# Performance work log

Hardware: AMD Instinct MI355X
Metric: run time of the kernel (lower is better)

Reference implementation:

```python
import jax, jax.numpy as jnp
import numpy as np

B, T, E = 512, 12, 1024   # batch, channels/seq, embed_dim
NH, HS = 8, 128           # num_heads, head_size (head_size=128 hard-coded in source)
H = NH * HS               # sLSTM hidden = 1024 (== E)


def _layer_norm(x, g, b, eps=1e-5):
    mu = x.mean(-1, keepdims=True)
    var = x.var(-1, keepdims=True)
    return (x - mu) * jax.lax.rsqrt(var + eps) * g + b


def _conv1d_same(x, w, b):
    # x: (B, C, L), w: (O, I, K) odd K, 'same' padding, stride 1
    k = w.shape[-1]
    p = (k - 1) // 2
    y = jax.lax.conv_general_dilated(x, w, (1,), [(p, p)],
                                     dimension_numbers=('NCH', 'OIH', 'NCH'))
    return y + b[None, :, None]


def setup_inputs():
    key = jax.random.key(0)
    ks = jax.random.split(key, 16)
    s = 0.02
    def nrm(k, shape, scale=s):
        return jax.random.normal(k, shape, jnp.float32) * scale
    return {
        'x': jax.random.normal(ks[0], (B, T, E), jnp.float32),
        'ln_g': jnp.ones((E,), jnp.float32), 'ln_b': jnp.zeros((E,), jnp.float32),
        'fc1_w': nrm(ks[1], (12, 12, 3)), 'fc1_b': jnp.zeros((12,), jnp.float32),
        'fc2_w': nrm(ks[2], (12, 12)), 'fc2_b': jnp.zeros((12,), jnp.float32),
        'conv1_w': nrm(ks[3], (48, 12, 3)), 'conv1_b': jnp.zeros((48,), jnp.float32),
        'conv2_w': nrm(ks[4], (12, 48, 3)), 'conv2_b': jnp.zeros((12,), jnp.float32),
        'xl_ln_g': jnp.ones((E,), jnp.float32), 'xl_ln_b': jnp.zeros((E,), jnp.float32),
        'Wg': nrm(ks[5], (E, 4 * H)), 'bg': jnp.zeros((4 * H,), jnp.float32),
        'Rg': nrm(ks[6], (NH, 4 * HS, HS)),
        'gn_g': jnp.ones((H,), jnp.float32), 'gn_b': jnp.zeros((H,), jnp.float32),
        'upl_w': nrm(ks[7], (H, H)), 'upl_b': jnp.zeros((H,), jnp.float32),
        'upr_w': nrm(ks[8], (H, H)), 'upr_b': jnp.zeros((H,), jnp.float32),
        'down_w': nrm(ks[9], (H, E)), 'down_b': jnp.zeros((E,), jnp.float32),
    }


def _slstm_block(x, xl_ln_g, xl_ln_b, Wg, bg, Rg, gn_g, gn_b,
                 upl_w, upl_b, upr_w, upr_b, down_w, down_b):
    # Stabilized multi-head sLSTM block: pre-LN -> sLSTM recurrence (exp i/f gates
    # with max-stabilizer m), per-head GroupNorm, gated up/down proj (proj_factor=1),
    # residual. Recurrent weights are block-diagonal per head (NH, 4*HS, HS).
    xn = _layer_norm(x, xl_ln_g, xl_ln_b)
    gx = jnp.einsum('bte,eg->btg', xn, Wg) + bg            # (B,T,4H) input gate pre-acts
    gx = jnp.swapaxes(gx, 0, 1)                            # (T,B,4H)

    def step(carry, g_t):
        h, c, n, m = carry                                 # each (B,NH,HS)
        rec = jnp.einsum('bnh,ngh->bng', h, Rg)            # (B,NH,4HS)
        g = g_t.reshape(g_t.shape[0], NH, 4 * HS) + rec
        z_, i_, f_, o_ = jnp.split(g, 4, axis=-1)
        z = jnp.tanh(z_)
        o = jax.nn.sigmoid(o_)
        m_new = jnp.maximum(f_ + m, i_)                    # log-space stabilizer
        i = jnp.exp(i_ - m_new)
        f = jnp.exp(f_ + m - m_new)
        c = f * c + i * z
        n = f * n + i
        h = o * (c / n)
        return (h, c, n, m_new), h

    zero = jnp.zeros((x.shape[0], NH, HS), x.dtype)
    _, hseq = jax.lax.scan(step, (zero, zero, zero, zero), gx)
    h = jnp.swapaxes(hseq, 0, 1)                           # (B,T,NH,HS)
    # GroupNorm(num_groups=NH) over each head's HS channels
    mu = h.mean(-1, keepdims=True)
    var = h.var(-1, keepdims=True)
    hn = (h - mu) * jax.lax.rsqrt(var + 1e-5)
    hn = hn.reshape(x.shape[0], x.shape[1], H) * gn_g + gn_b
    left = jax.nn.gelu(hn @ upl_w + upl_b, approximate=False)
    right = hn @ upr_w + upr_b
    return (left * right) @ down_w + down_b + x


def reference(x, ln_g, ln_b, fc1_w, fc1_b, fc2_w, fc2_b, conv1_w, conv1_b,
              conv2_w, conv2_b, xl_ln_g, xl_ln_b, Wg, bg, Rg, gn_g, gn_b,
              upl_w, upl_b, upr_w, upr_b, down_w, down_b):
    xn = _layer_norm(x, ln_g, ln_b)
    skip = xn
    xc = _conv1d_same(xn, fc1_w, fc1_b)                    # fc1: Conv1d(12,12,3,'same')
    x1 = jnp.einsum('bcl,oc->bol', xc, fc2_w) + fc2_b[None, :, None]  # fc2: 1x1 conv
    x1 = _slstm_block(x1, xl_ln_g, xl_ln_b, Wg, bg, Rg, gn_g, gn_b,
                      upl_w, upl_b, upr_w, upr_b, down_w, down_b)
    # dropout(0.2) is identity in eval mode
    y = jax.nn.silu(xc) * x1 + skip
    z = _conv1d_same(y, conv1_w, conv1_b)                  # 12 -> 48
    z = _layer_norm(jax.nn.gelu(z, approximate=False), ln_g, ln_b)
    z = _conv1d_same(z, conv2_w, conv2_b)                  # 48 -> 12
    return z + skip
```

## Files before the change

kernel.cpp:

```cpp
#include <hip/hip_runtime.h>
#include <math.h>


typedef short short8_t __attribute__((ext_vector_type(8)));
typedef float floatx4 __attribute__((ext_vector_type(4)));
typedef float float4_t __attribute__((ext_vector_type(4)));

typedef unsigned int u32;
typedef const __attribute__((address_space(1))) u32 gu32;
typedef __attribute__((address_space(3))) u32 lu32;

static __device__ __forceinline__ float b2f(unsigned short u) {
    unsigned v = ((unsigned)u) << 16;
    return __builtin_bit_cast(float, v);
}
static __device__ __forceinline__ unsigned short f2b(float f) {
    unsigned u = __builtin_bit_cast(unsigned, f);
    u += 0x7FFFu + ((u >> 16) & 1u);
    return (unsigned short)(u >> 16);
}
static __device__ __forceinline__ float gelu_exact(float x) {
    return 0.5f * x * (1.f + erff(x * 0.70710678118654752f));
}


__global__ __launch_bounds__(256) void transpose_bf16_k(
    const float* __restrict__ src, unsigned short* __restrict__ dst, int K, int N)
{
    __shared__ unsigned short tl[32][33];
    const int n0 = blockIdx.x * 32, k0 = blockIdx.y * 32;
    const int tx = threadIdx.x & 31, ty = threadIdx.x >> 5;
#pragma unroll
    for (int r = 0; r < 4; r++) {
        int k = ty + r * 8;
        tl[tx][k] = f2b(src[(size_t)(k0 + k) * N + n0 + tx]);
    }
    __syncthreads();
#pragma unroll
    for (int r = 0; r < 4; r++) {
        int n = ty * 4 + r;
        dst[(size_t)(n0 + n) * K + k0 + tx] = tl[n][tx];
    }
}

__global__ __launch_bounds__(256) void cat_bias_k(
    const float* __restrict__ a, const float* __restrict__ b, float* __restrict__ o)
{
    int gid = blockIdx.x * 256 + threadIdx.x;
    o[gid] = (gid < 1024) ? a[gid] : b[gid - 1024];
}


template <int BF16OUT>
__global__ __launch_bounds__(256) void ln_kernel(
    const float* __restrict__ in, const float* __restrict__ g,
    const float* __restrict__ be, void* __restrict__ outp)
{
    const int row = blockIdx.x;
    const float* xr = in + (size_t)row * 1024;
    const int t = threadIdx.x;
    float v[4];
    float s = 0.f, ss = 0.f;
#pragma unroll
    for (int u = 0; u < 4; u++) {
        float q = xr[t + u * 256];
        v[u] = q; s += q; ss += q * q;
    }
#pragma unroll
    for (int off = 32; off >= 1; off >>= 1) {
        s += __shfl_xor(s, off);
        ss += __shfl_xor(ss, off);
    }
    __shared__ float red[8];
    const int wv = t >> 6, la = t & 63;
    if (la == 0) { red[wv] = s; red[4 + wv] = ss; }
    __syncthreads();
    s = red[0] + red[1] + red[2] + red[3];
    ss = red[4] + red[5] + red[6] + red[7];
    float mu = s * (1.f / 1024.f);
    float var = ss * (1.f / 1024.f) - mu * mu;
    float rs = rsqrtf(var + 1e-5f);
#pragma unroll
    for (int u = 0; u < 4; u++) {
        int i = t + u * 256;
        float yv = (v[u] - mu) * rs * g[i] + be[i];
        if (BF16OUT)
            ((unsigned short*)outp)[(size_t)row * 1024 + i] = f2b(yv);
        else
            ((float*)outp)[(size_t)row * 1024 + i] = yv;
    }
}


__global__ __launch_bounds__(256) void fc_kernel(
    const float* __restrict__ xn,
    const float* __restrict__ w1, const float* __restrict__ b1,
    const float* __restrict__ w2, const float* __restrict__ b2,
    float* __restrict__ xc, float* __restrict__ x1)
{
    const int t = threadIdx.x;
    const int gid = blockIdx.x * 256 + t;
    const int b = gid >> 10, l = gid & 1023;
    const float* xb = xn + (size_t)b * 12288;
    float inm[12], in0[12], inp[12];
#pragma unroll
    for (int ci = 0; ci < 12; ci++) {
        in0[ci] = xb[ci * 1024 + l];
        inm[ci] = (l > 0) ? xb[ci * 1024 + l - 1] : 0.f;
        inp[ci] = (l < 1023) ? xb[ci * 1024 + l + 1] : 0.f;
    }
    float xcv[12];
#pragma unroll
    for (int o = 0; o < 12; o++) {
        float a = b1[o];
#pragma unroll
        for (int ci = 0; ci < 12; ci++) {
            const float* wp = w1 + o * 36 + ci * 3;
            a += inm[ci] * wp[0] + in0[ci] * wp[1] + inp[ci] * wp[2];
        }
        xcv[o] = a;
        xc[(size_t)b * 12288 + o * 1024 + l] = a;
    }
#pragma unroll
    for (int o = 0; o < 12; o++) {
        float a = b2[o];
#pragma unroll
        for (int ci = 0; ci < 12; ci++) a += xcv[ci] * w2[o * 12 + ci];
        x1[(size_t)b * 12288 + o * 1024 + l] = a;
    }
}


template <int MODE>
__global__ __launch_bounds__(256) void gemm_kernel(
    const unsigned short* __restrict__ A, const unsigned short* __restrict__ BT,
    const float* __restrict__ bias, void* __restrict__ out,
    int M, int N, int K,
    const float* __restrict__ xc, const float* __restrict__ x1,
    const float* __restrict__ skip)
{
    __shared__ __align__(16) unsigned short sA[128 * 32];
    __shared__ __align__(16) unsigned short sB[128 * 32];
    const int t = threadIdx.x;
    const int m0 = blockIdx.y * 128;
    const int n0 = blockIdx.x * 128;
    const int w = t >> 6;
    const int lane = t & 63;
    const int wr = (w >> 1) * 64;
    const int wc = (w & 1) * 64;
    const int lrow = lane & 15;
    const int quad = lane >> 4;
    const int row_l = t >> 2;
    const int cs = (t & 3) * 8;

    const unsigned short* gA0 = A + (size_t)(m0 + row_l) * K + cs;
    const unsigned short* gA1 = A + (size_t)(m0 + row_l + 64) * K + cs;
    const unsigned short* gB0 = BT + (size_t)(n0 + row_l) * K + cs;
    const unsigned short* gB1 = BT + (size_t)(n0 + row_l + 64) * K + cs;
    unsigned short* lA0 = sA + w * 512;
    unsigned short* lA1 = sA + 2048 + w * 512;
    unsigned short* lB0 = sB + w * 512;
    unsigned short* lB1 = sB + 2048 + w * 512;

    floatx4 acc[4][4];
#pragma unroll
    for (int i = 0; i < 4; i++)
#pragma unroll
        for (int j = 0; j < 4; j++) acc[i][j] = (floatx4)0.f;

    for (int k0 = 0; k0 < K; k0 += 32) {
        __syncthreads();
        __builtin_amdgcn_global_load_lds((gu32*)(gA0 + k0), (lu32*)lA0, 16, 0, 0);
        __builtin_amdgcn_global_load_lds((gu32*)(gA1 + k0), (lu32*)lA1, 16, 0, 0);
        __builtin_amdgcn_global_load_lds((gu32*)(gB0 + k0), (lu32*)lB0, 16, 0, 0);
        __builtin_amdgcn_global_load_lds((gu32*)(gB1 + k0), (lu32*)lB1, 16, 0, 0);
        __syncthreads();
        short8_t af[4], bfr[4];
#pragma unroll
        for (int i = 0; i < 4; i++) {
            af[i] = *(const short8_t*)(sA + (wr + i * 16 + lrow) * 32 + quad * 8);
            bfr[i] = *(const short8_t*)(sB + (wc + i * 16 + lrow) * 32 + quad * 8);
        }
#pragma unroll
        for (int i = 0; i < 4; i++)
#pragma unroll
            for (int j = 0; j < 4; j++)
                acc[i][j] = __builtin_amdgcn_mfma_f32_16x16x32_bf16(
                    af[i], bfr[j], acc[i][j], 0, 0, 0);
    }

#pragma unroll
    for (int i = 0; i < 4; i++) {
#pragma unroll
        for (int j = 0; j < 4; j++) {
#pragma unroll
            for (int r = 0; r < 4; r++) {
                const int gm = m0 + wr + i * 16 + quad * 4 + r;
                const int gn = n0 + wc + j * 16 + lrow;
                const size_t idx = (size_t)gm * N + gn;
                float v = acc[i][j][r] + bias[gn];
                if (MODE == 0) {
                    ((unsigned short*)out)[idx] = f2b(v);
                } else {
                    float xcv = xc[idx];
                    float sig = xcv / (1.f + __expf(-xcv));
                    ((float*)out)[idx] = sig * (v + x1[idx]) + skip[idx];
                }
            }
        }
    }
}


#define RECP 516
#define HBP  136

__global__ __launch_bounds__(1024, 4) void slstm_rec_kernel(
    const float* __restrict__ Rg,
    const unsigned short* __restrict__ gxb,
    const float* __restrict__ gn_g, const float* __restrict__ gn_b,
    unsigned short* __restrict__ hnb)
{
    __shared__ __align__(16) float sRec[16 * RECP];
    __shared__ __align__(16) unsigned short sHb[16 * HBP];
    const int head = blockIdx.x;
    const int b0 = blockIdx.y * 16;
    const int t = threadIdx.x;
    const int w = t >> 6;
    const int lane = t & 63;
    const int quad = lane >> 4;
    const int l16 = lane & 15;

    short8_t Bf[2][4];
    {
        const float* Rh = Rg + (size_t)head * 65536;
#pragma unroll
        for (int jt = 0; jt < 2; jt++)
#pragma unroll
            for (int kk = 0; kk < 4; kk++) {
                const float* src =
                    Rh + (size_t)(w * 32 + jt * 16 + l16) * 128 + kk * 32 + quad * 8;
                short8_t v;
#pragma unroll
                for (int j = 0; j < 8; j++) v[j] = (short)f2b(src[j]);
                Bf[jt][kk] = v;
            }
    }

    for (int i = t; i < 16 * HBP; i += 1024) sHb[i] = 0;

    const int la = lane;
    float c0 = 0.f, n0s = 0.f, m0 = 0.f;
    float c1 = 0.f, n1s = 0.f, m1 = 0.f;
    const float gg0 = gn_g[head * 128 + la];
    const float gg1 = gn_g[head * 128 + la + 64];
    const float gb0 = gn_b[head * 128 + la];
    const float gb1 = gn_b[head * 128 + la + 64];

    __syncthreads();

    for (int step = 0; step < 12; step++) {
        const unsigned short* gp =
            gxb + ((size_t)(b0 + w) * 12 + step) * 4096 + head * 512;
        float gz0 = b2f(gp[la]),       gz1 = b2f(gp[64 + la]);
        float gi0 = b2f(gp[128 + la]), gi1 = b2f(gp[192 + la]);
        float gf0 = b2f(gp[256 + la]), gf1 = b2f(gp[320 + la]);
        float go0 = b2f(gp[384 + la]), go1 = b2f(gp[448 + la]);

        short8_t Af[4];
#pragma unroll
        for (int kk = 0; kk < 4; kk++)
            Af[kk] = *(const short8_t*)(sHb + l16 * HBP + kk * 32 + quad * 8);
        floatx4 D0 = (floatx4)0.f, D1 = (floatx4)0.f;
#pragma unroll
        for (int kk = 0; kk < 4; kk++) {
            D0 = __builtin_amdgcn_mfma_f32_16x16x32_bf16(Af[kk], Bf[0][kk], D0, 0, 0, 0);
            D1 = __builtin_amdgcn_mfma_f32_16x16x32_bf16(Af[kk], Bf[1][kk], D1, 0, 0, 0);
        }
#pragma unroll
        for (int r = 0; r < 4; r++) {
            sRec[(quad * 4 + r) * RECP + w * 32 + l16] = D0[r];
            sRec[(quad * 4 + r) * RECP + w * 32 + 16 + l16] = D1[r];
        }
        __syncthreads();

        const float* rr = sRec + w * RECP;
        float zp0 = gz0 + rr[la],       zp1 = gz1 + rr[64 + la];
        float ip0 = gi0 + rr[128 + la], ip1 = gi1 + rr[192 + la];
        float fp0 = gf0 + rr[256 + la], fp1 = gf1 + rr[320 + la];
        float op0 = go0 + rr[384 + la], op1 = go1 + rr[448 + la];

        float e20 = __expf(2.f * zp0), e21 = __expf(2.f * zp1);
        float z0 = (e20 - 1.f) / (e20 + 1.f), z1 = (e21 - 1.f) / (e21 + 1.f);
        float o0 = 1.f / (1.f + __expf(-op0)), o1 = 1.f / (1.f + __expf(-op1));
        float mn0 = fmaxf(fp0 + m0, ip0), mn1 = fmaxf(fp1 + m1, ip1);
        float ie0 = __expf(ip0 - mn0), ie1 = __expf(ip1 - mn1);
        float fe0 = __expf(fp0 + m0 - mn0), fe1 = __expf(fp1 + m1 - mn1);
        c0 = fe0 * c0 + ie0 * z0;  c1 = fe1 * c1 + ie1 * z1;
        n0s = fe0 * n0s + ie0;     n1s = fe1 * n1s + ie1;
        m0 = mn0;                  m1 = mn1;
        float h0 = o0 * (c0 / n0s), h1 = o1 * (c1 / n1s);

        float s = h0 + h1, ss = h0 * h0 + h1 * h1;
#pragma unroll
        for (int off = 32; off >= 1; off >>= 1) {
            s += __shfl_xor(s, off);
            ss += __shfl_xor(ss, off);
        }
        float mu = s * (1.f / 128.f);
        float var = ss * (1.f / 128.f) - mu * mu;
        float rs = rsqrtf(var + 1e-5f);
        size_t base = ((size_t)(b0 + w) * 12 + step) * 1024 + head * 128;
        hnb[base + la] = f2b((h0 - mu) * rs * gg0 + gb0);
        hnb[base + la + 64] = f2b((h1 - mu) * rs * gg1 + gb1);

        sHb[w * HBP + la] = f2b(h0);
        sHb[w * HBP + la + 64] = f2b(h1);
        __syncthreads();
    }
}


__global__ __launch_bounds__(256) void gate_kernel(
    const unsigned short* __restrict__ lr, unsigned short* __restrict__ glr)
{
    size_t gid = (size_t)blockIdx.x * 256 + threadIdx.x;
    size_t m = gid >> 10;
    int j = (int)(gid & 1023);
    float lf = b2f(lr[m * 2048 + j]);
    float rt = b2f(lr[m * 2048 + 1024 + j]);
    glr[gid] = f2b(gelu_exact(lf) * rt);
}


__global__ __launch_bounds__(1024, 4) void tail_fused_kernel(
    const float* __restrict__ y, const float* __restrict__ skip,
    const float* __restrict__ w1, const float* __restrict__ b1,
    const float* __restrict__ w2, const float* __restrict__ b2,
    const float* __restrict__ lng, const float* __restrict__ lnb,
    float* __restrict__ out)
{
    __shared__ unsigned short sY[12][1032];
    __shared__ unsigned short sZ[48][1032];
    __shared__ float sLg[1024], sLb[1024];
    __shared__ float sMR[48][2];
    const int b = blockIdx.x;
    const int t = threadIdx.x;

    {
        const float* yb = y + (size_t)b * 12288;
#pragma unroll
        for (int r = 0; r < 12; r++) sY[r][t] = f2b(yb[r * 1024 + t]);
    }
    sLg[t] = lng[t];
    sLb[t] = lnb[t];
    __syncthreads();

    float vm[12], v0[12], vp[12];
#pragma unroll
    for (int ci = 0; ci < 12; ci++) {
        v0[ci] = b2f(sY[ci][t]);
        vm[ci] = (t > 0) ? b2f(sY[ci][t - 1]) : 0.f;
        vp[ci] = (t < 1023) ? b2f(sY[ci][t + 1]) : 0.f;
    }
    for (int o = 0; o < 48; o++) {
        const float* wp = w1 + o * 36;
        float a = b1[o];
#pragma unroll
        for (int ci = 0; ci < 12; ci++)
            a += vm[ci] * wp[ci * 3] + v0[ci] * wp[ci * 3 + 1] + vp[ci] * wp[ci * 3 + 2];
        sZ[o][t] = f2b(gelu_exact(a));
    }
    __syncthreads();

    {
        const int w = t >> 6, la = t & 63;
        for (int o = w * 3; o < w * 3 + 3; o++) {
            float s = 0.f, ss = 0.f;
#pragma unroll
            for (int u = 0; u < 16; u++) {
                float v = b2f(sZ[o][la + u * 64]);
                s += v; ss += v * v;
            }
#pragma unroll
            for (int off = 32; off >= 1; off >>= 1) {
                s += __shfl_xor(s, off);
                ss += __shfl_xor(ss, off);
            }
            if (la == 0) {
                float mu = s * (1.f / 1024.f);
                float var = ss * (1.f / 1024.f) - mu * mu;
                sMR[o][0] = mu;
                sMR[o][1] = rsqrtf(var + 1e-5f);
            }
        }
    }
    __syncthreads();

    float acc[12];
#pragma unroll
    for (int o = 0; o < 12; o++) acc[o] = b2[o];
    const float lg0 = sLg[t], lb0 = sLb[t];
    const float lgm = (t > 0) ? sLg[t - 1] : 0.f;
    const float lbm = (t > 0) ? sLb[t - 1] : 0.f;
    const float lgp = (t < 1023) ? sLg[t + 1] : 0.f;
    const float lbp = (t < 1023) ? sLb[t + 1] : 0.f;
    for (int ci = 0; ci < 48; ci++) {
        const float mu = sMR[ci][0], rs = sMR[ci][1];
        float znm = (t > 0) ? ((b2f(sZ[ci][t - 1]) - mu) * rs * lgm + lbm) : 0.f;
        float zn0 = (b2f(sZ[ci][t]) - mu) * rs * lg0 + lb0;
        float znp = (t < 1023) ? ((b2f(sZ[ci][t + 1]) - mu) * rs * lgp + lbp) : 0.f;
        const float* wp = w2 + ci * 3;
#pragma unroll
        for (int o = 0; o < 12; o++)
            acc[o] += znm * wp[o * 144] + zn0 * wp[o * 144 + 1] + znp * wp[o * 144 + 2];
    }
    const size_t base = (size_t)b * 12288 + t;
#pragma unroll
    for (int o = 0; o < 12; o++) {
        size_t idx = base + (size_t)o * 1024;
        out[idx] = acc[o] + skip[idx];
    }
}


extern "C" void kernel_launch(void* const* d_in, const int* in_sizes, int n_in,
                              void* d_out, int out_size, void* d_ws, size_t ws_size,
                              hipStream_t stream)
{
    (void)in_sizes; (void)n_in; (void)out_size; (void)ws_size;
    const float* x      = (const float*)d_in[0];
    const float* ln_g   = (const float*)d_in[1];
    const float* ln_b   = (const float*)d_in[2];
    const float* fc1_w  = (const float*)d_in[3];
    const float* fc1_b  = (const float*)d_in[4];
    const float* fc2_w  = (const float*)d_in[5];
    const float* fc2_b  = (const float*)d_in[6];
    const float* conv1_w= (const float*)d_in[7];
    const float* conv1_b= (const float*)d_in[8];
    const float* conv2_w= (const float*)d_in[9];
    const float* conv2_b= (const float*)d_in[10];
    const float* xl_g   = (const float*)d_in[11];
    const float* xl_b   = (const float*)d_in[12];
    const float* Wg     = (const float*)d_in[13];
    const float* bg     = (const float*)d_in[14];
    const float* Rg     = (const float*)d_in[15];
    const float* gn_g   = (const float*)d_in[16];
    const float* gn_b   = (const float*)d_in[17];
    const float* upl_w  = (const float*)d_in[18];
    const float* upl_b  = (const float*)d_in[19];
    const float* upr_w  = (const float*)d_in[20];
    const float* upr_b  = (const float*)d_in[21];
    const float* down_w = (const float*)d_in[22];
    const float* down_b = (const float*)d_in[23];

    char* ws = (char*)d_ws;
    size_t off = 0;
    auto alloc = [&](size_t bytes) -> char* {
        char* p = ws + off;
        off = (off + bytes + 255) & ~(size_t)255;
        return p;
    };
    float* xn            = (float*)alloc(25165824);
    float* xc            = (float*)alloc(25165824);
    float* x1            = (float*)alloc(25165824);
    unsigned short* xn2b = (unsigned short*)alloc(12582912);
    unsigned short* gxb  = (unsigned short*)alloc(50331648);
    unsigned short* hnb  = (unsigned short*)alloc(12582912);
    unsigned short* lrb  = (unsigned short*)alloc(25165824);
    unsigned short* glrb = (unsigned short*)alloc(12582912);
    float* yb            = (float*)alloc(25165824);
    unsigned short* WgT  = (unsigned short*)alloc(8388608);
    unsigned short* WupT = (unsigned short*)alloc(4194304);
    unsigned short* WdT  = (unsigned short*)alloc(2097152);
    float* bup           = (float*)alloc(8192);

    transpose_bf16_k<<<dim3(128, 32), 256, 0, stream>>>(Wg, WgT, 1024, 4096);
    transpose_bf16_k<<<dim3(32, 32), 256, 0, stream>>>(upl_w, WupT, 1024, 1024);
    transpose_bf16_k<<<dim3(32, 32), 256, 0, stream>>>(upr_w, WupT + 1024 * 1024, 1024, 1024);
    transpose_bf16_k<<<dim3(32, 32), 256, 0, stream>>>(down_w, WdT, 1024, 1024);
    cat_bias_k<<<8, 256, 0, stream>>>(upl_b, upr_b, bup);

    ln_kernel<0><<<6144, 256, 0, stream>>>(x, ln_g, ln_b, xn);
    fc_kernel<<<2048, 256, 0, stream>>>(xn, fc1_w, fc1_b, fc2_w, fc2_b, xc, x1);
    ln_kernel<1><<<6144, 256, 0, stream>>>(x1, xl_g, xl_b, xn2b);
    gemm_kernel<0><<<dim3(32, 48), 256, 0, stream>>>(
        xn2b, WgT, bg, gxb, 6144, 4096, 1024, nullptr, nullptr, nullptr);
    slstm_rec_kernel<<<dim3(8, 32), 1024, 0, stream>>>(Rg, gxb, gn_g, gn_b, hnb);
    gemm_kernel<0><<<dim3(16, 48), 256, 0, stream>>>(
        hnb, WupT, bup, lrb, 6144, 2048, 1024, nullptr, nullptr, nullptr);
    gate_kernel<<<24576, 256, 0, stream>>>(lrb, glrb);
    gemm_kernel<2><<<dim3(8, 48), 256, 0, stream>>>(
        glrb, WdT, down_b, yb, 6144, 1024, 1024, xc, x1, xn);
    tail_fused_kernel<<<512, 1024, 0, stream>>>(
        yb, xn, conv1_w, conv1_b, conv2_w, conv2_b, ln_g, ln_b, (float*)d_out);
}
```

Before: 482.4 us.

## Fuse up-projection GEMMs with GELU gate, bf16 y, restructure tail conv kernel

```diff
diff --git a/kernel.cpp b/kernel.cpp
--- a/kernel.cpp
+++ b/kernel.cpp
@@ -4,7 +4,7 @@
 
 typedef short short8_t __attribute__((ext_vector_type(8)));
 typedef float floatx4 __attribute__((ext_vector_type(4)));
-typedef float float4_t __attribute__((ext_vector_type(4)));
+typedef float float2_t __attribute__((ext_vector_type(2)));
 
 typedef unsigned int u32;
 typedef const __attribute__((address_space(1))) u32 gu32;
@@ -19,8 +19,21 @@
     u += 0x7FFFu + ((u >> 16) & 1u);
     return (unsigned short)(u >> 16);
 }
+static __device__ __forceinline__ float2_t make2u(unsigned u) {
+    float2_t r;
+    r.x = __builtin_bit_cast(float, u << 16);
+    r.y = __builtin_bit_cast(float, u & 0xFFFF0000u);
+    return r;
+}
 static __device__ __forceinline__ float gelu_exact(float x) {
     return 0.5f * x * (1.f + erff(x * 0.70710678118654752f));
+}
+static __device__ __forceinline__ float gelu_fast(float x) {
+    float u = 0.7978845608f * x * (1.f + 0.044715f * x * x);
+    u = fminf(fmaxf(u, -9.f), 9.f);
+    float e = __expf(2.f * u);
+    float t = (e - 1.f) / (e + 1.f);
+    return 0.5f * x * (1.f + t);
 }
 
 
@@ -41,13 +54,6 @@
         int n = ty * 4 + r;
         dst[(size_t)(n0 + n) * K + k0 + tx] = tl[n][tx];
     }
-}
-
-__global__ __launch_bounds__(256) void cat_bias_k(
-    const float* __restrict__ a, const float* __restrict__ b, float* __restrict__ o)
-{
-    int gid = blockIdx.x * 256 + threadIdx.x;
-    o[gid] = (gid < 1024) ? a[gid] : b[gid - 1024];
 }
 
 
@@ -204,8 +210,92 @@
                 } else {
                     float xcv = xc[idx];
                     float sig = xcv / (1.f + __expf(-xcv));
-                    ((float*)out)[idx] = sig * (v + x1[idx]) + skip[idx];
+                    ((unsigned short*)out)[idx] =
+                        f2b(sig * (v + x1[idx]) + skip[idx]);
                 }
+            }
+        }
+    }
+}
+
+
+__global__ __launch_bounds__(256) void gemm_upgate_kernel(
+    const unsigned short* __restrict__ A, const unsigned short* __restrict__ BT,
+    const float* __restrict__ lbias, const float* __restrict__ rbias,
+    unsigned short* __restrict__ glr, int K)
+{
+    __shared__ __align__(16) unsigned short sA[128 * 32];
+    __shared__ __align__(16) unsigned short sL[128 * 32];
+    __shared__ __align__(16) unsigned short sR[128 * 32];
+    const int t = threadIdx.x;
+    const int m0 = blockIdx.y * 128;
+    const int n0 = blockIdx.x * 128;
+    const int w = t >> 6;
+    const int lane = t & 63;
+    const int wr = (w >> 1) * 64;
+    const int wc = (w & 1) * 64;
+    const int lrow = lane & 15;
+    const int quad = lane >> 4;
+    const int row_l = t >> 2;
+    const int cs = (t & 3) * 8;
+
+    const unsigned short* gA0 = A + (size_t)(m0 + row_l) * K + cs;
+    const unsigned short* gA1 = A + (size_t)(m0 + row_l + 64) * K + cs;
+    const unsigned short* gL0 = BT + (size_t)(n0 + row_l) * K + cs;
+    const unsigned short* gL1 = BT + (size_t)(n0 + row_l + 64) * K + cs;
+    const unsigned short* gR0 = BT + (size_t)(1024 + n0 + row_l) * K + cs;
+    const unsigned short* gR1 = BT + (size_t)(1024 + n0 + row_l + 64) * K + cs;
+    unsigned short* lA0 = sA + w * 512;
+    unsigned short* lA1 = sA + 2048 + w * 512;
+    unsigned short* lL0 = sL + w * 512;
+    unsigned short* lL1 = sL + 2048 + w * 512;
+    unsigned short* lR0 = sR + w * 512;
+    unsigned short* lR1 = sR + 2048 + w * 512;
+
+    floatx4 accL[4][4], accR[4][4];
+#pragma unroll
+    for (int i = 0; i < 4; i++)
+#pragma unroll
+        for (int j = 0; j < 4; j++) { accL[i][j] = (floatx4)0.f; accR[i][j] = (floatx4)0.f; }
+
+    for (int k0 = 0; k0 < K; k0 += 32) {
+        __syncthreads();
+        __builtin_amdgcn_global_load_lds((gu32*)(gA0 + k0), (lu32*)lA0, 16, 0, 0);
+        __builtin_amdgcn_global_load_lds((gu32*)(gA1 + k0), (lu32*)lA1, 16, 0, 0);
+        __builtin_amdgcn_global_load_lds((gu32*)(gL0 + k0), (lu32*)lL0, 16, 0, 0);
+        __builtin_amdgcn_global_load_lds((gu32*)(gL1 + k0), (lu32*)lL1, 16, 0, 0);
+        __builtin_amdgcn_global_load_lds((gu32*)(gR0 + k0), (lu32*)lR0, 16, 0, 0);
+        __builtin_amdgcn_global_load_lds((gu32*)(gR1 + k0), (lu32*)lR1, 16, 0, 0);
+        __syncthreads();
+        short8_t af[4], bl[4], br[4];
+#pragma unroll
+        for (int i = 0; i < 4; i++) {
+            af[i] = *(const short8_t*)(sA + (wr + i * 16 + lrow) * 32 + quad * 8);
+            bl[i] = *(const short8_t*)(sL + (wc + i * 16 + lrow) * 32 + quad * 8);
+            br[i] = *(const short8_t*)(sR + (wc + i * 16 + lrow) * 32 + quad * 8);
+        }
+#pragma unroll
+        for (int i = 0; i < 4; i++)
+#pragma unroll
+            for (int j = 0; j < 4; j++) {
+                accL[i][j] = __builtin_amdgcn_mfma_f32_16x16x32_bf16(
+                    af[i], bl[j], accL[i][j], 0, 0, 0);
+                accR[i][j] = __builtin_amdgcn_mfma_f32_16x16x32_bf16(
+                    af[i], br[j], accR[i][j], 0, 0, 0);
+            }
+    }
+
+#pragma unroll
+    for (int i = 0; i < 4; i++) {
+#pragma unroll
+        for (int j = 0; j < 4; j++) {
+#pragma unroll
+            for (int r = 0; r < 4; r++) {
+                const int gm = m0 + wr + i * 16 + quad * 4 + r;
+                const int gn = n0 + wc + j * 16 + lrow;
+                float lv = accL[i][j][r] + lbias[gn];
+                float rv = accR[i][j][r] + rbias[gn];
+                glr[(size_t)gm * 1024 + gn] = f2b(gelu_exact(lv) * rv);
             }
         }
     }
@@ -321,105 +411,117 @@
 }
 
 
-__global__ __launch_bounds__(256) void gate_kernel(
-    const unsigned short* __restrict__ lr, unsigned short* __restrict__ glr)
-{
-    size_t gid = (size_t)blockIdx.x * 256 + threadIdx.x;
-    size_t m = gid >> 10;
-    int j = (int)(gid & 1023);
-    float lf = b2f(lr[m * 2048 + j]);
-    float rt = b2f(lr[m * 2048 + 1024 + j]);
-    glr[gid] = f2b(gelu_exact(lf) * rt);
-}
-
-
-__global__ __launch_bounds__(1024, 4) void tail_fused_kernel(
-    const float* __restrict__ y, const float* __restrict__ skip,
+__global__ __launch_bounds__(512, 4) void tail_fused_kernel(
+    const unsigned short* __restrict__ y, const float* __restrict__ skip,
     const float* __restrict__ w1, const float* __restrict__ b1,
     const float* __restrict__ w2, const float* __restrict__ b2,
     const float* __restrict__ lng, const float* __restrict__ lnb,
     float* __restrict__ out)
 {
     __shared__ unsigned short sY[12][1032];
-    __shared__ unsigned short sZ[48][1032];
-    __shared__ float sLg[1024], sLb[1024];
-    __shared__ float sMR[48][2];
+    __shared__ unsigned short sZ[24][1032];
+    __shared__ float sMR[24][2];
     const int b = blockIdx.x;
     const int t = threadIdx.x;
+    const int p0 = 2 * t;
+    const size_t boff = (size_t)b * 12288;
 
     {
-        const float* yb = y + (size_t)b * 12288;
-#pragma unroll
-        for (int r = 0; r < 12; r++) sY[r][t] = f2b(yb[r * 1024 + t]);
-    }
-    sLg[t] = lng[t];
-    sLb[t] = lnb[t];
+        const u32* gy = (const u32*)(y + boff);
+#pragma unroll
+        for (int ci = 0; ci < 12; ci++)
+            ((u32*)&sY[ci][0])[t] = gy[ci * 512 + t];
+    }
+    const float lg0 = lng[p0], lb0 = lnb[p0];
+    const float lg1 = lng[p0 + 1], lb1 = lnb[p0 + 1];
+    const float lgm = (t > 0) ? lng[p0 - 1] : 0.f;
+    const float lbm = (t > 0) ? lnb[p0 - 1] : 0.f;
+    const float lgp = (t < 511) ? lng[p0 + 2] : 0.f;
+    const float lbp = (t < 511) ? lnb[p0 + 2] : 0.f;
     __syncthreads();
 
-    float vm[12], v0[12], vp[12];
-#pragma unroll
-    for (int ci = 0; ci < 12; ci++) {
-        v0[ci] = b2f(sY[ci][t]);
-        vm[ci] = (t > 0) ? b2f(sY[ci][t - 1]) : 0.f;
-        vp[ci] = (t < 1023) ? b2f(sY[ci][t + 1]) : 0.f;
-    }
-    for (int o = 0; o < 48; o++) {
-        const float* wp = w1 + o * 36;
-        float a = b1[o];
-#pragma unroll
-        for (int ci = 0; ci < 12; ci++)
-            a += vm[ci] * wp[ci * 3] + v0[ci] * wp[ci * 3 + 1] + vp[ci] * wp[ci * 3 + 2];
-        sZ[o][t] = f2b(gelu_exact(a));
-    }
-    __syncthreads();
-
-    {
-        const int w = t >> 6, la = t & 63;
-        for (int o = w * 3; o < w * 3 + 3; o++) {
-            float s = 0.f, ss = 0.f;
-#pragma unroll
-            for (int u = 0; u < 16; u++) {
-                float v = b2f(sZ[o][la + u * 64]);
-                s += v; ss += v * v;
+    float2_t acc[12];
+#pragma unroll
+    for (int o = 0; o < 12; o++) { float bv = b2[o]; acc[o] = float2_t{bv, bv}; }
+
+    for (int half = 0; half < 2; half++) {
+        float2_t a1[24];
+#pragma unroll
+        for (int o = 0; o < 24; o++) {
+            float bo = b1[half * 24 + o];
+            a1[o] = float2_t{bo, bo};
+        }
+        for (int ci = 0; ci < 12; ci++) {
+            u32 pr = *(const u32*)(&sY[ci][p0]);
+            float2_t c = make2u(pr);
+            float ym = (t > 0) ? b2f(sY[ci][p0 - 1]) : 0.f;
+            float yp = (t < 511) ? b2f(sY[ci][p0 + 2]) : 0.f;
+            float2_t vm = float2_t{ym, c.x};
+            float2_t vp = float2_t{c.y, yp};
+            const float* wp = w1 + half * 24 * 36 + ci * 3;
+#pragma unroll
+            for (int o = 0; o < 24; o++)
+                a1[o] += vm * wp[o * 36] + c * wp[o * 36 + 1] + vp * wp[o * 36 + 2];
+        }
+#pragma unroll
+        for (int o = 0; o < 24; o++) {
+            u32 pz = ((u32)f2b(gelu_fast(a1[o].y)) << 16) | f2b(gelu_fast(a1[o].x));
+            *(u32*)(&sZ[o][p0]) = pz;
+        }
+        __syncthreads();
+
+        {
+            const int wv = t >> 6, la = t & 63;
+#pragma unroll
+            for (int j = 0; j < 3; j++) {
+                const int ch = wv + j * 8;
+                float s = 0.f, ss = 0.f;
+#pragma unroll
+                for (int u = 0; u < 8; u++) {
+                    float2_t v = make2u(((const u32*)&sZ[ch][0])[la + u * 64]);
+                    s += v.x + v.y;
+                    ss += v.x * v.x + v.y * v.y;
+                }
+#pragma unroll
+                for (int off = 32; off >= 1; off >>= 1) {
+                    s += __shfl_xor(s, off);
+                    ss += __shfl_xor(ss, off);
+                }
+                if (la == 0) {
+                    float mu = s * (1.f / 1024.f);
+                    float var = ss * (1.f / 1024.f) - mu * mu;
+                    sMR[ch][0] = mu;
+                    sMR[ch][1] = rsqrtf(var + 1e-5f);
+                }
             }
-#pragma unroll
-            for (int off = 32; off >= 1; off >>= 1) {
-                s += __shfl_xor(s, off);
-                ss += __shfl_xor(ss, off);
-            }
-            if (la == 0) {
-                float mu = s * (1.f / 1024.f);
-                float var = ss * (1.f / 1024.f) - mu * mu;
-                sMR[o][0] = mu;
-                sMR[o][1] = rsqrtf(var + 1e-5f);
-            }
-        }
-    }
-    __syncthreads();
-
-    float acc[12];
-#pragma unroll
-    for (int o = 0; o < 12; o++) acc[o] = b2[o];
-    const float lg0 = sLg[t], lb0 = sLb[t];
-    const float lgm = (t > 0) ? sLg[t - 1] : 0.f;
-    const float lbm = (t > 0) ? sLb[t - 1] : 0.f;
-    const float lgp = (t < 1023) ? sLg[t + 1] : 0.f;
-    const float lbp = (t < 1023) ? sLb[t + 1] : 0.f;
-    for (int ci = 0; ci < 48; ci++) {
-        const float mu = sMR[ci][0], rs = sMR[ci][1];
-        float znm = (t > 0) ? ((b2f(sZ[ci][t - 1]) - mu) * rs * lgm + lbm) : 0.f;
-        float zn0 = (b2f(sZ[ci][t]) - mu) * rs * lg0 + lb0;
-        float znp = (t < 1023) ? ((b2f(sZ[ci][t + 1]) - mu) * rs * lgp + lbp) : 0.f;
-        const float* wp = w2 + ci * 3;
-#pragma unroll
-        for (int o = 0; o < 12; o++)
-            acc[o] += znm * wp[o * 144] + zn0 * wp[o * 144 + 1] + znp * wp[o * 144 + 2];
-    }
-    const size_t base = (size_t)b * 12288 + t;
+        }
+        __syncthreads();
+
+        for (int ci = 0; ci < 24; ci++) {
+            const float mu = sMR[ci][0], rs = sMR[ci][1];
+            u32 pr = *(const u32*)(&sZ[ci][p0]);
+            float2_t c = make2u(pr);
+            float zmr = (t > 0) ? b2f(sZ[ci][p0 - 1]) : 0.f;
+            float zpr = (t < 511) ? b2f(sZ[ci][p0 + 2]) : 0.f;
+            float2_t z0 = float2_t{(c.x - mu) * rs * lg0 + lb0,
+                                   (c.y - mu) * rs * lg1 + lb1};
+            float2_t zm = float2_t{(t > 0) ? ((zmr - mu) * rs * lgm + lbm) : 0.f,
+                                   z0.x};
+            float2_t zp = float2_t{z0.y,
+                                   (t < 511) ? ((zpr - mu) * rs * lgp + lbp) : 0.f};
+            const float* wp = w2 + (half * 24 + ci) * 3;
+#pragma unroll
+            for (int o = 0; o < 12; o++)
+                acc[o] += zm * wp[o * 144] + z0 * wp[o * 144 + 1] + zp * wp[o * 144 + 2];
+        }
+        __syncthreads();
+    }
+
 #pragma unroll
     for (int o = 0; o < 12; o++) {
-        size_t idx = base + (size_t)o * 1024;
-        out[idx] = acc[o] + skip[idx];
+        size_t i0 = boff + (size_t)o * 1024 + p0;
+        float2_t sk = *(const float2_t*)(&skip[i0]);
+        *(float2_t*)(&out[i0]) = acc[o] + sk;
     }
 }
 
@@ -467,19 +569,16 @@
     unsigned short* xn2b = (unsigned short*)alloc(12582912);
     unsigned short* gxb  = (unsigned short*)alloc(50331648);
     unsigned short* hnb  = (unsigned short*)alloc(12582912);
-    unsigned short* lrb  = (unsigned short*)alloc(25165824);
     unsigned short* glrb = (unsigned short*)alloc(12582912);
-    float* yb            = (float*)alloc(25165824);
+    unsigned short* yb   = (unsigned short*)alloc(12582912);
     unsigned short* WgT  = (unsigned short*)alloc(8388608);
     unsigned short* WupT = (unsigned short*)alloc(4194304);
     unsigned short* WdT  = (unsigned short*)alloc(2097152);
-    float* bup           = (float*)alloc(8192);
 
     transpose_bf16_k<<<dim3(128, 32), 256, 0, stream>>>(Wg, WgT, 1024, 4096);
     transpose_bf16_k<<<dim3(32, 32), 256, 0, stream>>>(upl_w, WupT, 1024, 1024);
     transpose_bf16_k<<<dim3(32, 32), 256, 0, stream>>>(upr_w, WupT + 1024 * 1024, 1024, 1024);
     transpose_bf16_k<<<dim3(32, 32), 256, 0, stream>>>(down_w, WdT, 1024, 1024);
-    cat_bias_k<<<8, 256, 0, stream>>>(upl_b, upr_b, bup);
 
     ln_kernel<0><<<6144, 256, 0, stream>>>(x, ln_g, ln_b, xn);
     fc_kernel<<<2048, 256, 0, stream>>>(xn, fc1_w, fc1_b, fc2_w, fc2_b, xc, x1);
@@ -487,11 +586,10 @@
     gemm_kernel<0><<<dim3(32, 48), 256, 0, stream>>>(
         xn2b, WgT, bg, gxb, 6144, 4096, 1024, nullptr, nullptr, nullptr);
     slstm_rec_kernel<<<dim3(8, 32), 1024, 0, stream>>>(Rg, gxb, gn_g, gn_b, hnb);
-    gemm_kernel<0><<<dim3(16, 48), 256, 0, stream>>>(
-        hnb, WupT, bup, lrb, 6144, 2048, 1024, nullptr, nullptr, nullptr);
-    gate_kernel<<<24576, 256, 0, stream>>>(lrb, glrb);
+    gemm_upgate_kernel<<<dim3(8, 48), 256, 0, stream>>>(
+        hnb, WupT, upl_b, upr_b, glrb, 1024);
     gemm_kernel<2><<<dim3(8, 48), 256, 0, stream>>>(
         glrb, WdT, down_b, yb, 6144, 1024, 1024, xc, x1, xn);
-    tail_fused_kernel<<<512, 1024, 0, stream>>>(
+    tail_fused_kernel<<<512, 512, 0, stream>>>(
         yb, xn, conv1_w, conv1_b, conv2_w, conv2_b, ln_g, ln_b, (float*)d_out);
 }
```

New measurement: 514.8 us. +6.7%, slower.

## Restructure tail conv kernel, use fast tanh GELU, store y in bf16

Applied to the files above, without the earlier changes.

```diff
diff --git a/kernel.cpp b/kernel.cpp
--- a/kernel.cpp
+++ b/kernel.cpp
@@ -4,7 +4,7 @@
 
 typedef short short8_t __attribute__((ext_vector_type(8)));
 typedef float floatx4 __attribute__((ext_vector_type(4)));
-typedef float float4_t __attribute__((ext_vector_type(4)));
+typedef float float2_t __attribute__((ext_vector_type(2)));
 
 typedef unsigned int u32;
 typedef const __attribute__((address_space(1))) u32 gu32;
@@ -19,8 +19,21 @@
     u += 0x7FFFu + ((u >> 16) & 1u);
     return (unsigned short)(u >> 16);
 }
-static __device__ __forceinline__ float gelu_exact(float x) {
-    return 0.5f * x * (1.f + erff(x * 0.70710678118654752f));
+static __device__ __forceinline__ float2_t make2u(unsigned u) {
+    float2_t r;
+    r.x = __builtin_bit_cast(float, u << 16);
+    r.y = __builtin_bit_cast(float, u & 0xFFFF0000u);
+    return r;
+}
+static __device__ __forceinline__ u32 pack2(float a, float b) {
+    return ((u32)f2b(b) << 16) | (u32)f2b(a);
+}
+static __device__ __forceinline__ float gelu_fast(float x) {
+    float u = 0.7978845608f * x * (1.f + 0.044715f * x * x);
+    u = fminf(fmaxf(u, -9.f), 9.f);
+    float e = __expf(2.f * u);
+    float t = (e - 1.f) / (e + 1.f);
+    return 0.5f * x * (1.f + t);
 }
 
 
@@ -41,13 +54,6 @@
         int n = ty * 4 + r;
         dst[(size_t)(n0 + n) * K + k0 + tx] = tl[n][tx];
     }
-}
-
-__global__ __launch_bounds__(256) void cat_bias_k(
-    const float* __restrict__ a, const float* __restrict__ b, float* __restrict__ o)
-{
-    int gid = blockIdx.x * 256 + threadIdx.x;
-    o[gid] = (gid < 1024) ? a[gid] : b[gid - 1024];
 }
 
 
@@ -204,7 +210,8 @@
                 } else {
                     float xcv = xc[idx];
                     float sig = xcv / (1.f + __expf(-xcv));
-                    ((float*)out)[idx] = sig * (v + x1[idx]) + skip[idx];
+                    ((unsigned short*)out)[idx] =
+                        f2b(sig * (v + x1[idx]) + skip[idx]);
                 }
             }
         }
@@ -324,102 +331,130 @@
 __global__ __launch_bounds__(256) void gate_kernel(
     const unsigned short* __restrict__ lr, unsigned short* __restrict__ glr)
 {
-    size_t gid = (size_t)blockIdx.x * 256 + threadIdx.x;
-    size_t m = gid >> 10;
-    int j = (int)(gid & 1023);
-    float lf = b2f(lr[m * 2048 + j]);
-    float rt = b2f(lr[m * 2048 + 1024 + j]);
-    glr[gid] = f2b(gelu_exact(lf) * rt);
-}
-
-
-__global__ __launch_bounds__(1024, 4) void tail_fused_kernel(
-    const float* __restrict__ y, const float* __restrict__ skip,
+    u32 pi = blockIdx.x * 256 + threadIdx.x;
+    u32 m = pi >> 9, c = pi & 511;
+    const u32* row = (const u32*)(lr + (size_t)m * 2048);
+    float2_t lf = make2u(row[c]);
+    float2_t rt = make2u(row[512 + c]);
+    ((u32*)glr)[pi] = pack2(gelu_fast(lf.x) * rt.x, gelu_fast(lf.y) * rt.y);
+}
+
+
+__global__ __launch_bounds__(512, 6) void tail_fused_kernel(
+    const unsigned short* __restrict__ y, const float* __restrict__ skip,
     const float* __restrict__ w1, const float* __restrict__ b1,
     const float* __restrict__ w2, const float* __restrict__ b2,
     const float* __restrict__ lng, const float* __restrict__ lnb,
     float* __restrict__ out)
 {
-    __shared__ unsigned short sY[12][1032];
-    __shared__ unsigned short sZ[48][1032];
-    __shared__ float sLg[1024], sLb[1024];
-    __shared__ float sMR[48][2];
+    __shared__ unsigned short sY[12][1026];
+    __shared__ unsigned short sZ[12][1026];
+    __shared__ float sMR[12][2];
     const int b = blockIdx.x;
     const int t = threadIdx.x;
+    const int p = t;
+    const size_t boff = (size_t)b * 12288;
 
     {
-        const float* yb = y + (size_t)b * 12288;
-#pragma unroll
-        for (int r = 0; r < 12; r++) sY[r][t] = f2b(yb[r * 1024 + t]);
-    }
-    sLg[t] = lng[t];
-    sLb[t] = lnb[t];
+        const u32* gy = (const u32*)(y + boff);
+#pragma unroll
+        for (int ci = 0; ci < 12; ci++)
+            ((u32*)&sY[ci][0])[t] = gy[ci * 512 + t];
+    }
+    const float lgA = lng[2 * t], lbA = lnb[2 * t];
+    const float lgB = lng[2 * t + 1], lbB = lnb[2 * t + 1];
     __syncthreads();
 
-    float vm[12], v0[12], vp[12];
-#pragma unroll
-    for (int ci = 0; ci < 12; ci++) {
-        v0[ci] = b2f(sY[ci][t]);
-        vm[ci] = (t > 0) ? b2f(sY[ci][t - 1]) : 0.f;
-        vp[ci] = (t < 1023) ? b2f(sY[ci][t + 1]) : 0.f;
-    }
-    for (int o = 0; o < 48; o++) {
-        const float* wp = w1 + o * 36;
-        float a = b1[o];
-#pragma unroll
-        for (int ci = 0; ci < 12; ci++)
-            a += vm[ci] * wp[ci * 3] + v0[ci] * wp[ci * 3 + 1] + vp[ci] * wp[ci * 3 + 2];
-        sZ[o][t] = f2b(gelu_exact(a));
-    }
-    __syncthreads();
-
-    {
-        const int w = t >> 6, la = t & 63;
-        for (int o = w * 3; o < w * 3 + 3; o++) {
-            float s = 0.f, ss = 0.f;
-#pragma unroll
-            for (int u = 0; u < 16; u++) {
-                float v = b2f(sZ[o][la + u * 64]);
-                s += v; ss += v * v;
+    float2_t acc[12];
+#pragma unroll
+    for (int o = 0; o < 12; o++) { float bv = b2[o]; acc[o] = float2_t{bv, bv}; }
+
+    for (int q = 0; q < 4; q++) {
+        float2_t a1[12];
+#pragma unroll
+        for (int o = 0; o < 12; o++) {
+            float bo = b1[q * 12 + o];
+            a1[o] = float2_t{bo, bo};
+        }
+        for (int ci = 0; ci < 12; ci++) {
+            float2_t v0 = float2_t{b2f(sY[ci][p]), b2f(sY[ci][p + 512])};
+            float2_t vm = float2_t{(p > 0) ? b2f(sY[ci][p - 1]) : 0.f,
+                                   b2f(sY[ci][p + 511])};
+            float2_t vp = float2_t{b2f(sY[ci][p + 1]),
+                                   (p < 511) ? b2f(sY[ci][p + 513]) : 0.f};
+            const float* wp = w1 + ci * 3;
+#pragma unroll
+            for (int o = 0; o < 12; o++) {
+                const float* wo = wp + (q * 12 + o) * 36;
+                a1[o] += vm * wo[0] + v0 * wo[1] + vp * wo[2];
             }
-#pragma unroll
-            for (int off = 32; off >= 1; off >>= 1) {
-                s += __shfl_xor(s, off);
-                ss += __shfl_xor(ss, off);
+        }
+#pragma unroll
+        for (int o = 0; o < 12; o++) {
+            sZ[o][p] = f2b(gelu_fast(a1[o].x));
+            sZ[o][p + 512] = f2b(gelu_fast(a1[o].y));
+        }
+        __syncthreads();
+
+        {
+            const int wv = t >> 6, la = t & 63;
+#pragma unroll
+            for (int j = 0; j < 2; j++) {
+                const int ch = wv + j * 8;
+                if (ch < 12) {
+                    float s = 0.f, ss = 0.f;
+#pragma unroll
+                    for (int u = 0; u < 8; u++) {
+                        float2_t v = make2u(((const u32*)&sZ[ch][0])[la + u * 64]);
+                        s += v.x + v.y;
+                        ss += v.x * v.x + v.y * v.y;
+                    }
+#pragma unroll
+                    for (int off = 32; off >= 1; off >>= 1) {
+                        s += __shfl_xor(s, off);
+                        ss += __shfl_xor(ss, off);
+                    }
+                    if (la == 0) {
+                        float mu = s * (1.f / 1024.f);
+                        float var = ss * (1.f / 1024.f) - mu * mu;
+                        sMR[ch][0] = mu;
+                        sMR[ch][1] = rsqrtf(var + 1e-5f);
+                    }
+                }
             }
-            if (la == 0) {
-                float mu = s * (1.f / 1024.f);
-                float var = ss * (1.f / 1024.f) - mu * mu;
-                sMR[o][0] = mu;
-                sMR[o][1] = rsqrtf(var + 1e-5f);
-            }
-        }
-    }
-    __syncthreads();
-
-    float acc[12];
-#pragma unroll
-    for (int o = 0; o < 12; o++) acc[o] = b2[o];
-    const float lg0 = sLg[t], lb0 = sLb[t];
-    const float lgm = (t > 0) ? sLg[t - 1] : 0.f;
-    const float lbm = (t > 0) ? sLb[t - 1] : 0.f;
-    const float lgp = (t < 1023) ? sLg[t + 1] : 0.f;
-    const float lbp = (t < 1023) ? sLb[t + 1] : 0.f;
-    for (int ci = 0; ci < 48; ci++) {
-        const float mu = sMR[ci][0], rs = sMR[ci][1];
-        float znm = (t > 0) ? ((b2f(sZ[ci][t - 1]) - mu) * rs * lgm + lbm) : 0.f;
-        float zn0 = (b2f(sZ[ci][t]) - mu) * rs * lg0 + lb0;
-        float znp = (t < 1023) ? ((b2f(sZ[ci][t + 1]) - mu) * rs * lgp + lbp) : 0.f;
-        const float* wp = w2 + ci * 3;
-#pragma unroll
-        for (int o = 0; o < 12; o++)
-            acc[o] += znm * wp[o * 144] + zn0 * wp[o * 144 + 1] + znp * wp[o * 144 + 2];
-    }
-    const size_t base = (size_t)b * 12288 + t;
+        }
+        __syncthreads();
+
+#pragma unroll
+        for (int ch = 0; ch < 12; ch++) {
+            const float mu = sMR[ch][0], rs = sMR[ch][1];
+            float2_t f = make2u(((const u32*)&sZ[ch][0])[t]);
+            f.x = (f.x - mu) * rs * lgA + lbA;
+            f.y = (f.y - mu) * rs * lgB + lbB;
+            ((u32*)&sZ[ch][0])[t] = pack2(f.x, f.y);
+        }
+        __syncthreads();
+
+        for (int ci = 0; ci < 12; ci++) {
+            float2_t z0 = float2_t{b2f(sZ[ci][p]), b2f(sZ[ci][p + 512])};
+            float2_t zm = float2_t{(p > 0) ? b2f(sZ[ci][p - 1]) : 0.f,
+                                   b2f(sZ[ci][p + 511])};
+            float2_t zp = float2_t{b2f(sZ[ci][p + 1]),
+                                   (p < 511) ? b2f(sZ[ci][p + 513]) : 0.f};
+            const float* wp = w2 + (q * 12 + ci) * 3;
+#pragma unroll
+            for (int o = 0; o < 12; o++)
+                acc[o] += zm * wp[o * 144] + z0 * wp[o * 144 + 1]
+                        + zp * wp[o * 144 + 2];
+        }
+        __syncthreads();
+    }
+
 #pragma unroll
     for (int o = 0; o < 12; o++) {
-        size_t idx = base + (size_t)o * 1024;
-        out[idx] = acc[o] + skip[idx];
+        size_t i0 = boff + (size_t)o * 1024 + p;
+        out[i0] = acc[o].x + skip[i0];
+        out[i0 + 512] = acc[o].y + skip[i0 + 512];
     }
 }
 
@@ -469,7 +504,7 @@
     unsigned short* hnb  = (unsigned short*)alloc(12582912);
     unsigned short* lrb  = (unsigned short*)alloc(25165824);
     unsigned short* glrb = (unsigned short*)alloc(12582912);
-    float* yb            = (float*)alloc(25165824);
+    unsigned short* yb   = (unsigned short*)alloc(12582912);
     unsigned short* WgT  = (unsigned short*)alloc(8388608);
     unsigned short* WupT = (unsigned short*)alloc(4194304);
     unsigned short* WdT  = (unsigned short*)alloc(2097152);
@@ -479,7 +514,10 @@
     transpose_bf16_k<<<dim3(32, 32), 256, 0, stream>>>(upl_w, WupT, 1024, 1024);
     transpose_bf16_k<<<dim3(32, 32), 256, 0, stream>>>(upr_w, WupT + 1024 * 1024, 1024, 1024);
     transpose_bf16_k<<<dim3(32, 32), 256, 0, stream>>>(down_w, WdT, 1024, 1024);
-    cat_bias_k<<<8, 256, 0, stream>>>(upl_b, upr_b, bup);
+    {
+        hipMemcpyAsync(bup, upl_b, 4096, hipMemcpyDeviceToDevice, stream);
+        hipMemcpyAsync(bup + 1024, upr_b, 4096, hipMemcpyDeviceToDevice, stream);
+    }
 
     ln_kernel<0><<<6144, 256, 0, stream>>>(x, ln_g, ln_b, xn);
     fc_kernel<<<2048, 256, 0, stream>>>(xn, fc1_w, fc1_b, fc2_w, fc2_b, xc, x1);
@@ -489,9 +527,9 @@
     slstm_rec_kernel<<<dim3(8, 32), 1024, 0, stream>>>(Rg, gxb, gn_g, gn_b, hnb);
     gemm_kernel<0><<<dim3(16, 48), 256, 0, stream>>>(
         hnb, WupT, bup, lrb, 6144, 2048, 1024, nullptr, nullptr, nullptr);
-    gate_kernel<<<24576, 256, 0, stream>>>(lrb, glrb);
+    gate_kernel<<<12288, 256, 0, stream>>>(lrb, glrb);
     gemm_kernel<2><<<dim3(8, 48), 256, 0, stream>>>(
         glrb, WdT, down_b, yb, 6144, 1024, 1024, xc, x1, xn);
-    tail_fused_kernel<<<512, 1024, 0, stream>>>(
+    tail_fused_kernel<<<512, 512, 0, stream>>>(
         yb, xn, conv1_w, conv1_b, conv2_w, conv2_b, ln_g, ln_b, (float*)d_out);
 }
```

New measurement: 466.7 us. -3.3%, faster.
